# Kernel optimization log

Hardware: AMD Instinct MI355X
Metric: run time of the kernel (lower is better)

The kernel has to match this reference:

```python
import jax, jax.numpy as jnp
import numpy as np

NEG = -1e9


def setup_inputs() -> dict:
    key = jax.random.key(0)
    kq, kk, kv, ke = jax.random.split(key, 4)
    B, H, S, D = 4, 16, 2048, 64
    q = jax.random.normal(kq, (B, H, S, D), dtype=jnp.float32)
    k = jax.random.normal(kk, (B, H, S, D), dtype=jnp.float32)
    v = jax.random.normal(kv, (B, H, S, D), dtype=jnp.float32)
    event_length = jax.random.randint(ke, (B,), 0, S, dtype=jnp.int32)
    return {"q": q, "k": k, "v": v, "event_length": event_length}


def reference(q, k, v, event_length):
    B, H, S, D = q.shape
    scale = jnp.sqrt(jnp.asarray(D, dtype=jnp.float32))
    # [b,h,s,q] scores
    scores = jnp.einsum('bhsd,bhqd->bhsq', q, k) / scale
    idx = jnp.arange(S)
    el = event_length[:, None]  # [B,1]
    valid = idx[None, :] < el   # [B,S]
    # mask[b,s,q] = valid[b,s] & valid[b,q]; broadcast over heads
    mask = (valid[:, None, :, None] & valid[:, None, None, :])  # [B,1,S,S]
    scores = jnp.where(mask, scores, NEG)
    attn = jax.nn.softmax(scores, axis=-1)
    # dropout p=0.0 (eval): identity
    out = jnp.einsum('bhsq,bhqd->bhsd', attn, v)
    return out
```

## Files before the change

### kernel.cpp

```cpp
#include <hip/hip_runtime.h>
#include <hip/hip_bf16.h>


#define SQ 2048
#define DH 64
#define NBH 64
#define TK 64
#define LDE 72

typedef __attribute__((ext_vector_type(4))) float f32x4;
typedef __attribute__((ext_vector_type(8))) short bf16x8;
typedef __attribute__((ext_vector_type(4))) unsigned int u32x4;
typedef __attribute__((ext_vector_type(2))) unsigned int u32x2;

__device__ __forceinline__ unsigned int pk2(float lo, float hi) {
    __hip_bfloat162 h = __float22bfloat162_rn(float2{lo, hi});
    union { __hip_bfloat162 h; unsigned int u; } c; c.h = h;
    return c.u;
}

__global__ __launch_bounds__(256)
void meanv_k(const float* __restrict__ V, float* __restrict__ MV) {
    const int bh  = blockIdx.x >> 4;
    const int seg = blockIdx.x & 15;
    const float* vp = V + ((size_t)bh * SQ + (size_t)seg * 128) * DH;
    const int c = threadIdx.x & 15;
    const int r = threadIdx.x >> 4;
    const float* p = vp + (size_t)r * DH + c * 4;
    f32x4 s0 = *(const f32x4*)(p);
    f32x4 s1 = *(const f32x4*)(p + 16 * DH);
    f32x4 s2 = *(const f32x4*)(p + 32 * DH);
    f32x4 s3 = *(const f32x4*)(p + 48 * DH);
    s0 += *(const f32x4*)(p + 64 * DH);
    s1 += *(const f32x4*)(p + 80 * DH);
    s2 += *(const f32x4*)(p + 96 * DH);
    s3 += *(const f32x4*)(p + 112 * DH);
    f32x4 s = (s0 + s1) + (s2 + s3);
    __shared__ f32x4 red[16][16];
    red[r][c] = s;
    __syncthreads();
    if (threadIdx.x < 16) {
        f32x4 a = red[0][threadIdx.x];
        #pragma unroll
        for (int j = 1; j < 16; ++j) a += red[j][threadIdx.x];
        const float inv = 1.0f / (float)SQ;
        atomicAdd(&MV[bh * DH + threadIdx.x * 4 + 0], a[0] * inv);
        atomicAdd(&MV[bh * DH + threadIdx.x * 4 + 1], a[1] * inv);
        atomicAdd(&MV[bh * DH + threadIdx.x * 4 + 2], a[2] * inv);
        atomicAdd(&MV[bh * DH + threadIdx.x * 4 + 3], a[3] * inv);
    }
}

__global__ __launch_bounds__(256, 3)
void flash5(const float* __restrict__ Q, const float* __restrict__ K,
            const float* __restrict__ V, const int* __restrict__ EL,
            const float* __restrict__ MV, float* __restrict__ O,
            int* __restrict__ ticket) {
    const int t = threadIdx.x;

    {
        const int bh0    = blockIdx.x & (NBH - 1);
        const int qbase0 = (blockIdx.x >> 6) * 128;
        const int el0    = EL[bh0 >> 4];
        if (qbase0 >= el0) {
            float* Op = O + (size_t)bh0 * SQ * DH;
            const int c16 = t & 15, r0 = t >> 4;
            f32x4 mv = *(const f32x4*)(MV + bh0 * DH + c16 * 4);
            #pragma unroll
            for (int i = 0; i < 8; ++i)
                *(f32x4*)(Op + (size_t)(qbase0 + r0 + i * 16) * DH + c16 * 4) = mv;
        }
    }

    const int el0 = EL[0], el1 = EL[1], el2 = EL[2], el3 = EL[3];
    const int v0 = (el0 + 127) >> 7, v1 = (el1 + 127) >> 7;
    const int v2 = (el2 + 127) >> 7, v3 = (el3 + 127) >> 7;
    const int n0 = 16 * v0, n1 = n0 + 16 * v1, n2 = n1 + 16 * v2;
    const int nvalid = n2 + 16 * v3;

    __shared__ short Kb[TK][LDE];
    __shared__ short Vt[DH][LDE];
    __shared__ short Pl[4][32][LDE];
    __shared__ int item_s;

    const int wq = t >> 6, lane = t & 63, qd = lane >> 4, c = lane & 15;

    const int ksrow = t >> 2;
    const int ksdc  = t & 3;
    const int vpair = t & 31;
    const int vdg   = t >> 5;

    for (;;) {
        if (t == 0) item_s = atomicAdd(ticket, 1);
        __syncthreads();
        const int it = item_s;
        if (it >= nvalid) break;

        int b, u, vb, el;
        if      (it < n0) { b = 0; u = it;      vb = v0; el = el0; }
        else if (it < n1) { b = 1; u = it - n0; vb = v1; el = el1; }
        else if (it < n2) { b = 2; u = it - n1; vb = v2; el = el2; }
        else              { b = 3; u = it - n2; vb = v3; el = el3; }
        const int head  = u / vb;
        const int qt    = u - head * vb;
        const int bh    = b * 16 + head;
        const int qbase = qt * 128;

        const size_t base = (size_t)bh * SQ * DH;
        const float* Qp = Q + base;
        const float* Kp = K + base;
        const float* Vp = V + base;
        float* Op = O + base;

        const float sc = 0.125f * 1.44269504f;
        bf16x8 qf[2][2];
        #pragma unroll
        for (int nt = 0; nt < 2; ++nt) {
            const int row = qbase + wq * 32 + nt * 16 + c;
            #pragma unroll
            for (int kc = 0; kc < 2; ++kc) {
                const float* p = Qp + (size_t)row * DH + kc * 32 + qd * 8;
                f32x4 a  = *(const f32x4*)p;
                f32x4 bb = *(const f32x4*)(p + 4);
                u32x4 f;
                f[0] = pk2(a[0] * sc, a[1] * sc);
                f[1] = pk2(a[2] * sc, a[3] * sc);
                f[2] = pk2(bb[0] * sc, bb[1] * sc);
                f[3] = pk2(bb[2] * sc, bb[3] * sc);
                qf[nt][kc] = *(bf16x8*)&f;
            }
        }

        float l_[2] = {0.f, 0.f};
        f32x4 oacc[4][2];
        #pragma unroll
        for (int dt = 0; dt < 4; ++dt)
            #pragma unroll
            for (int nt = 0; nt < 2; ++nt)
                oacc[dt][nt] = (f32x4){0.f, 0.f, 0.f, 0.f};

        const int nkt = (el + TK - 1) / TK;

        f32x4 kg0, kg1, kg2, kg3, vg0, vg1, vg2, vg3;
        {
            const float* kp = Kp + (size_t)ksrow * DH + ksdc * 16;
            kg0 = *(const f32x4*)kp;
            kg1 = *(const f32x4*)(kp + 4);
            kg2 = *(const f32x4*)(kp + 8);
            kg3 = *(const f32x4*)(kp + 12);
            const float* vp0 = Vp + (size_t)(2 * vpair) * DH + vdg * 8;
            vg0 = *(const f32x4*)vp0;
            vg1 = *(const f32x4*)(vp0 + 4);
            vg2 = *(const f32x4*)(vp0 + DH);
            vg3 = *(const f32x4*)(vp0 + DH + 4);
        }

        for (int kt = 0; kt < nkt; ++kt) {
            const int k0 = kt * TK;

            __syncthreads();
            {
                u32x4 w0, w1;
                w0[0] = pk2(kg0[0], kg0[1]); w0[1] = pk2(kg0[2], kg0[3]);
                w0[2] = pk2(kg1[0], kg1[1]); w0[3] = pk2(kg1[2], kg1[3]);
                w1[0] = pk2(kg2[0], kg2[1]); w1[1] = pk2(kg2[2], kg2[3]);
                w1[2] = pk2(kg3[0], kg3[1]); w1[3] = pk2(kg3[2], kg3[3]);
                *(u32x4*)&Kb[ksrow][ksdc * 16]     = w0;
                *(u32x4*)&Kb[ksrow][ksdc * 16 + 8] = w1;
            }
            {
                #pragma unroll
                for (int i = 0; i < 4; ++i) {
                    *(unsigned int*)&Vt[vdg * 8 + i][2 * vpair]     = pk2(vg0[i], vg2[i]);
                    *(unsigned int*)&Vt[vdg * 8 + 4 + i][2 * vpair] = pk2(vg1[i], vg3[i]);
                }
            }
            __syncthreads();

            if (kt + 1 < nkt) {
                const int kn = k0 + TK;
                const float* kp = Kp + (size_t)(kn + ksrow) * DH + ksdc * 16;
                kg0 = *(const f32x4*)kp;
                kg1 = *(const f32x4*)(kp + 4);
                kg2 = *(const f32x4*)(kp + 8);
                kg3 = *(const f32x4*)(kp + 12);
                const float* vp0 = Vp + (size_t)(kn + 2 * vpair) * DH + vdg * 8;
                vg0 = *(const f32x4*)vp0;
                vg1 = *(const f32x4*)(vp0 + 4);
                vg2 = *(const f32x4*)(vp0 + DH);
                vg3 = *(const f32x4*)(vp0 + DH + 4);
            }

            f32x4 st[4][2];
            #pragma unroll
            for (int mt = 0; mt < 4; ++mt) {
                bf16x8 a0 = *(const bf16x8*)&Kb[mt * 16 + c][qd * 8];
                bf16x8 a1 = *(const bf16x8*)&Kb[mt * 16 + c][32 + qd * 8];
                #pragma unroll
                for (int nt = 0; nt < 2; ++nt) {
                    f32x4 acc = (f32x4){0.f, 0.f, 0.f, 0.f};
                    acc = __builtin_amdgcn_mfma_f32_16x16x32_bf16(a0, qf[nt][0], acc, 0, 0, 0);
                    acc = __builtin_amdgcn_mfma_f32_16x16x32_bf16(a1, qf[nt][1], acc, 0, 0, 0);
                    st[mt][nt] = acc;
                }
            }

            if (k0 + TK > el) {
                #pragma unroll
                for (int mt = 0; mt < 4; ++mt)
                    #pragma unroll
                    for (int r = 0; r < 4; ++r)
                        if (k0 + mt * 16 + qd * 4 + r >= el) {
                            st[mt][0][r] = -1e30f;
                            st[mt][1][r] = -1e30f;
                        }
            }

            #pragma unroll
            for (int nt = 0; nt < 2; ++nt) {
                #pragma unroll
                for (int mt = 0; mt < 4; ++mt) {
                    const float p0 = exp2f(st[mt][nt][0]);
                    const float p1 = exp2f(st[mt][nt][1]);
                    const float p2 = exp2f(st[mt][nt][2]);
                    const float p3 = exp2f(st[mt][nt][3]);
                    l_[nt] += (p0 + p1) + (p2 + p3);
                    u32x2 pw;
                    pw[0] = pk2(p0, p1);
                    pw[1] = pk2(p2, p3);
                    *(u32x2*)&Pl[wq][nt * 16 + c][mt * 16 + qd * 4] = pw;
                }
            }

            #pragma unroll
            for (int kc = 0; kc < 2; ++kc) {
                bf16x8 pb0 = *(const bf16x8*)&Pl[wq][c][kc * 32 + qd * 8];
                bf16x8 pb1 = *(const bf16x8*)&Pl[wq][16 + c][kc * 32 + qd * 8];
                #pragma unroll
                for (int dt = 0; dt < 4; ++dt) {
                    bf16x8 vf = *(const bf16x8*)&Vt[dt * 16 + c][kc * 32 + qd * 8];
                    oacc[dt][0] = __builtin_amdgcn_mfma_f32_16x16x32_bf16(vf, pb0, oacc[dt][0], 0, 0, 0);
                    oacc[dt][1] = __builtin_amdgcn_mfma_f32_16x16x32_bf16(vf, pb1, oacc[dt][1], 0, 0, 0);
                }
            }
        }

        #pragma unroll
        for (int nt = 0; nt < 2; ++nt) {
            l_[nt] += __shfl_xor(l_[nt], 16);
            l_[nt] += __shfl_xor(l_[nt], 32);
        }

        #pragma unroll
        for (int nt = 0; nt < 2; ++nt) {
            const int row = qbase + wq * 32 + nt * 16 + c;
            if (row < el) {
                const float inv = 1.0f / l_[nt];
                #pragma unroll
                for (int dt = 0; dt < 4; ++dt) {
                    f32x4 o = oacc[dt][nt];
                    o[0] *= inv; o[1] *= inv; o[2] *= inv; o[3] *= inv;
                    *(f32x4*)(Op + (size_t)row * DH + dt * 16 + qd * 4) = o;
                }
            } else {
                #pragma unroll
                for (int dt = 0; dt < 4; ++dt) {
                    f32x4 mv = *(const f32x4*)(MV + bh * DH + dt * 16 + qd * 4);
                    *(f32x4*)(Op + (size_t)row * DH + dt * 16 + qd * 4) = mv;
                }
            }
        }
    }
}

extern "C" void kernel_launch(void* const* d_in, const int* in_sizes, int n_in,
                              void* d_out, int out_size, void* d_ws, size_t ws_size,
                              hipStream_t stream) {
    const float* q  = (const float*)d_in[0];
    const float* k  = (const float*)d_in[1];
    const float* v  = (const float*)d_in[2];
    const int*   el = (const int*)d_in[3];
    float* out = (float*)d_out;
    float* mv  = (float*)d_ws;
    int*   tk  = (int*)((char*)d_ws + NBH * DH * sizeof(float));

    hipMemsetAsync(d_ws, 0, NBH * DH * sizeof(float) + 64, stream);
    meanv_k<<<dim3(NBH * 16), dim3(256), 0, stream>>>(v, mv);
    flash5<<<dim3(NBH * (SQ / 128)), dim3(256), 0, stream>>>(q, k, v, el, mv, out, tk);
}
```

Baseline: 203.3 us.

## Pre-convert K and transpose V to bf16, use single-wave blocks loading fragments directly

Adds separate pre-pass kernels that convert K to bf16 and transpose V to bf16 in a workspace, with the V mean folded into the transpose pass. The attention kernel becomes a single 64-thread wave per 32-query tile that loads MFMA fragments straight from global memory. P stays in registers instead of round-tripping through LDS, which removes all shared memory and block barriers. The cost is extra global traffic and launches for the pre-pass, loss of K/V reuse across the four waves of the old block, and a fallback path without a work ticket when the workspace is small.

```diff
diff --git a/kernel.cpp b/kernel.cpp
--- a/kernel.cpp
+++ b/kernel.cpp
@@ -6,7 +6,6 @@
 #define DH 64
 #define NBH 64
 #define TK 64
-#define LDE 72
 
 typedef __attribute__((ext_vector_type(4))) float f32x4;
 typedef __attribute__((ext_vector_type(8))) short bf16x8;
@@ -20,81 +19,95 @@
 }
 
 __global__ __launch_bounds__(256)
-void meanv_k(const float* __restrict__ V, float* __restrict__ MV) {
-    const int bh  = blockIdx.x >> 4;
-    const int seg = blockIdx.x & 15;
-    const float* vp = V + ((size_t)bh * SQ + (size_t)seg * 128) * DH;
-    const int c = threadIdx.x & 15;
-    const int r = threadIdx.x >> 4;
-    const float* p = vp + (size_t)r * DH + c * 4;
-    f32x4 s0 = *(const f32x4*)(p);
-    f32x4 s1 = *(const f32x4*)(p + 16 * DH);
-    f32x4 s2 = *(const f32x4*)(p + 32 * DH);
-    f32x4 s3 = *(const f32x4*)(p + 48 * DH);
-    s0 += *(const f32x4*)(p + 64 * DH);
-    s1 += *(const f32x4*)(p + 80 * DH);
-    s2 += *(const f32x4*)(p + 96 * DH);
-    s3 += *(const f32x4*)(p + 112 * DH);
-    f32x4 s = (s0 + s1) + (s2 + s3);
-    __shared__ f32x4 red[16][16];
-    red[r][c] = s;
-    __syncthreads();
-    if (threadIdx.x < 16) {
-        f32x4 a = red[0][threadIdx.x];
-        #pragma unroll
-        for (int j = 1; j < 16; ++j) a += red[j][threadIdx.x];
+void convert_k(const float* __restrict__ K, unsigned int* __restrict__ Kb) {
+    const size_t i = ((size_t)blockIdx.x * 256 + threadIdx.x) * 16;
+    const float* p = K + i;
+    f32x4 a = *(const f32x4*)p;
+    f32x4 b = *(const f32x4*)(p + 4);
+    f32x4 c = *(const f32x4*)(p + 8);
+    f32x4 d = *(const f32x4*)(p + 12);
+    u32x4 o0, o1;
+    o0[0] = pk2(a[0], a[1]); o0[1] = pk2(a[2], a[3]);
+    o0[2] = pk2(b[0], b[1]); o0[3] = pk2(b[2], b[3]);
+    o1[0] = pk2(c[0], c[1]); o1[1] = pk2(c[2], c[3]);
+    o1[2] = pk2(d[0], d[1]); o1[3] = pk2(d[2], d[3]);
+    *(u32x4*)(Kb + i / 2)     = o0;
+    *(u32x4*)(Kb + i / 2 + 4) = o1;
+}
+
+__global__ __launch_bounds__(256)
+void transpose_v(const float* __restrict__ V, short* __restrict__ Vt,
+                 float* __restrict__ MV) {
+    const int bh = blockIdx.x >> 5;
+    const int k0 = (blockIdx.x & 31) * 64;
+    const int t  = threadIdx.x;
+    const int kb = t & 15;
+    const int dg = t >> 4;
+    const float* vp = V + ((size_t)bh * SQ + k0 + kb * 4) * DH + dg * 4;
+    f32x4 r0 = *(const f32x4*)vp;
+    f32x4 r1 = *(const f32x4*)(vp + DH);
+    f32x4 r2 = *(const f32x4*)(vp + 2 * DH);
+    f32x4 r3 = *(const f32x4*)(vp + 3 * DH);
+    short* op = Vt + ((size_t)bh * DH + dg * 4) * SQ + k0 + kb * 4;
+    #pragma unroll
+    for (int i = 0; i < 4; ++i) {
+        u32x2 w; w[0] = pk2(r0[i], r1[i]); w[1] = pk2(r2[i], r3[i]);
+        *(u32x2*)(op + (size_t)i * SQ) = w;
+    }
+    f32x4 s = r0 + r1 + r2 + r3;
+    #pragma unroll
+    for (int d = 1; d < 16; d <<= 1) {
+        s[0] += __shfl_xor(s[0], d);
+        s[1] += __shfl_xor(s[1], d);
+        s[2] += __shfl_xor(s[2], d);
+        s[3] += __shfl_xor(s[3], d);
+    }
+    if ((t & 15) == 0) {
         const float inv = 1.0f / (float)SQ;
-        atomicAdd(&MV[bh * DH + threadIdx.x * 4 + 0], a[0] * inv);
-        atomicAdd(&MV[bh * DH + threadIdx.x * 4 + 1], a[1] * inv);
-        atomicAdd(&MV[bh * DH + threadIdx.x * 4 + 2], a[2] * inv);
-        atomicAdd(&MV[bh * DH + threadIdx.x * 4 + 3], a[3] * inv);
-    }
-}
-
-__global__ __launch_bounds__(256, 3)
-void flash5(const float* __restrict__ Q, const float* __restrict__ K,
-            const float* __restrict__ V, const int* __restrict__ EL,
+        atomicAdd(&MV[bh * DH + dg * 4 + 0], s[0] * inv);
+        atomicAdd(&MV[bh * DH + dg * 4 + 1], s[1] * inv);
+        atomicAdd(&MV[bh * DH + dg * 4 + 2], s[2] * inv);
+        atomicAdd(&MV[bh * DH + dg * 4 + 3], s[3] * inv);
+    }
+}
+
+__global__ __launch_bounds__(64, 3)
+void flash6(const float* __restrict__ Q, const short* __restrict__ Kg,
+            const short* __restrict__ Vg, const int* __restrict__ EL,
             const float* __restrict__ MV, float* __restrict__ O,
             int* __restrict__ ticket) {
-    const int t = threadIdx.x;
+    const int lane = threadIdx.x;
+    const int qd = lane >> 4, c = lane & 15;
 
     {
-        const int bh0    = blockIdx.x & (NBH - 1);
-        const int qbase0 = (blockIdx.x >> 6) * 128;
-        const int el0    = EL[bh0 >> 4];
-        if (qbase0 >= el0) {
+        const int bh0 = blockIdx.x & (NBH - 1);
+        const int qb0 = (blockIdx.x >> 6) * 32;
+        if (qb0 >= EL[bh0 >> 4]) {
             float* Op = O + (size_t)bh0 * SQ * DH;
-            const int c16 = t & 15, r0 = t >> 4;
-            f32x4 mv = *(const f32x4*)(MV + bh0 * DH + c16 * 4);
+            f32x4 mv = *(const f32x4*)(MV + bh0 * DH + c * 4);
             #pragma unroll
             for (int i = 0; i < 8; ++i)
-                *(f32x4*)(Op + (size_t)(qbase0 + r0 + i * 16) * DH + c16 * 4) = mv;
+                *(f32x4*)(Op + (size_t)(qb0 + qd + i * 4) * DH + c * 4) = mv;
         }
     }
 
     const int el0 = EL[0], el1 = EL[1], el2 = EL[2], el3 = EL[3];
-    const int v0 = (el0 + 127) >> 7, v1 = (el1 + 127) >> 7;
-    const int v2 = (el2 + 127) >> 7, v3 = (el3 + 127) >> 7;
+    const int v0 = (el0 + 31) >> 5, v1 = (el1 + 31) >> 5;
+    const int v2 = (el2 + 31) >> 5, v3 = (el3 + 31) >> 5;
     const int n0 = 16 * v0, n1 = n0 + 16 * v1, n2 = n1 + 16 * v2;
     const int nvalid = n2 + 16 * v3;
-
-    __shared__ short Kb[TK][LDE];
-    __shared__ short Vt[DH][LDE];
-    __shared__ short Pl[4][32][LDE];
-    __shared__ int item_s;
-
-    const int wq = t >> 6, lane = t & 63, qd = lane >> 4, c = lane & 15;
-
-    const int ksrow = t >> 2;
-    const int ksdc  = t & 3;
-    const int vpair = t & 31;
-    const int vdg   = t >> 5;
+    const float sc = 0.125f * 1.44269504f;
 
     for (;;) {
-        if (t == 0) item_s = atomicAdd(ticket, 1);
-        __syncthreads();
-        const int it = item_s;
-        if (it >= nvalid) break;
+        int it;
+        if (ticket) {
+            if (lane == 0) it = atomicAdd(ticket, 1);
+            it = __shfl(it, 0);
+            if (it >= nvalid) break;
+        } else {
+            it = blockIdx.x;
+            if (it >= nvalid) break;
+        }
 
         int b, u, vb, el;
         if      (it < n0) { b = 0; u = it;      vb = v0; el = el0; }
@@ -102,21 +115,19 @@
         else if (it < n2) { b = 2; u = it - n1; vb = v2; el = el2; }
         else              { b = 3; u = it - n2; vb = v3; el = el3; }
         const int head  = u / vb;
-        const int qt    = u - head * vb;
+        const int qc    = u - head * vb;
         const int bh    = b * 16 + head;
-        const int qbase = qt * 128;
-
-        const size_t base = (size_t)bh * SQ * DH;
-        const float* Qp = Q + base;
-        const float* Kp = K + base;
-        const float* Vp = V + base;
-        float* Op = O + base;
-
-        const float sc = 0.125f * 1.44269504f;
+        const int qbase = qc * 32;
+
+        const float* Qp = Q + (size_t)bh * SQ * DH;
+        const short* Kp = Kg + (size_t)bh * SQ * DH;
+        const short* Vp = Vg + (size_t)bh * DH * SQ;
+        float* Op = O + (size_t)bh * SQ * DH;
+
         bf16x8 qf[2][2];
         #pragma unroll
         for (int nt = 0; nt < 2; ++nt) {
-            const int row = qbase + wq * 32 + nt * 16 + c;
+            const int row = qbase + nt * 16 + c;
             #pragma unroll
             for (int kc = 0; kc < 2; ++kc) {
                 const float* p = Qp + (size_t)row * DH + kc * 32 + qd * 8;
@@ -140,70 +151,39 @@
                 oacc[dt][nt] = (f32x4){0.f, 0.f, 0.f, 0.f};
 
         const int nkt = (el + TK - 1) / TK;
-
-        f32x4 kg0, kg1, kg2, kg3, vg0, vg1, vg2, vg3;
-        {
-            const float* kp = Kp + (size_t)ksrow * DH + ksdc * 16;
-            kg0 = *(const f32x4*)kp;
-            kg1 = *(const f32x4*)(kp + 4);
-            kg2 = *(const f32x4*)(kp + 8);
-            kg3 = *(const f32x4*)(kp + 12);
-            const float* vp0 = Vp + (size_t)(2 * vpair) * DH + vdg * 8;
-            vg0 = *(const f32x4*)vp0;
-            vg1 = *(const f32x4*)(vp0 + 4);
-            vg2 = *(const f32x4*)(vp0 + DH);
-            vg3 = *(const f32x4*)(vp0 + DH + 4);
-        }
-
         for (int kt = 0; kt < nkt; ++kt) {
             const int k0 = kt * TK;
 
-            __syncthreads();
-            {
-                u32x4 w0, w1;
-                w0[0] = pk2(kg0[0], kg0[1]); w0[1] = pk2(kg0[2], kg0[3]);
-                w0[2] = pk2(kg1[0], kg1[1]); w0[3] = pk2(kg1[2], kg1[3]);
-                w1[0] = pk2(kg2[0], kg2[1]); w1[1] = pk2(kg2[2], kg2[3]);
-                w1[2] = pk2(kg3[0], kg3[1]); w1[3] = pk2(kg3[2], kg3[3]);
-                *(u32x4*)&Kb[ksrow][ksdc * 16]     = w0;
-                *(u32x4*)&Kb[ksrow][ksdc * 16 + 8] = w1;
-            }
-            {
-                #pragma unroll
-                for (int i = 0; i < 4; ++i) {
-                    *(unsigned int*)&Vt[vdg * 8 + i][2 * vpair]     = pk2(vg0[i], vg2[i]);
-                    *(unsigned int*)&Vt[vdg * 8 + 4 + i][2 * vpair] = pk2(vg1[i], vg3[i]);
-                }
-            }
-            __syncthreads();
-
-            if (kt + 1 < nkt) {
-                const int kn = k0 + TK;
-                const float* kp = Kp + (size_t)(kn + ksrow) * DH + ksdc * 16;
-                kg0 = *(const f32x4*)kp;
-                kg1 = *(const f32x4*)(kp + 4);
-                kg2 = *(const f32x4*)(kp + 8);
-                kg3 = *(const f32x4*)(kp + 12);
-                const float* vp0 = Vp + (size_t)(kn + 2 * vpair) * DH + vdg * 8;
-                vg0 = *(const f32x4*)vp0;
-                vg1 = *(const f32x4*)(vp0 + 4);
-                vg2 = *(const f32x4*)(vp0 + DH);
-                vg3 = *(const f32x4*)(vp0 + DH + 4);
+            bf16x8 kf[4][2];
+            #pragma unroll
+            for (int mt = 0; mt < 4; ++mt) {
+                const short* kp = Kp + (size_t)(k0 + mt * 16 + c) * DH + qd * 8;
+                kf[mt][0] = *(const bf16x8*)kp;
+                kf[mt][1] = *(const bf16x8*)(kp + 32);
+            }
+            u32x4 vf[4][2];
+            #pragma unroll
+            for (int dt = 0; dt < 4; ++dt) {
+                const short* vp = Vp + (size_t)(dt * 16 + c) * SQ + k0 + qd * 4;
+                #pragma unroll
+                for (int kc = 0; kc < 2; ++kc) {
+                    u32x2 aa = *(const u32x2*)(vp + kc * 32);
+                    u32x2 bb = *(const u32x2*)(vp + kc * 32 + 16);
+                    vf[dt][kc][0] = aa[0]; vf[dt][kc][1] = aa[1];
+                    vf[dt][kc][2] = bb[0]; vf[dt][kc][3] = bb[1];
+                }
             }
 
             f32x4 st[4][2];
             #pragma unroll
-            for (int mt = 0; mt < 4; ++mt) {
-                bf16x8 a0 = *(const bf16x8*)&Kb[mt * 16 + c][qd * 8];
-                bf16x8 a1 = *(const bf16x8*)&Kb[mt * 16 + c][32 + qd * 8];
+            for (int mt = 0; mt < 4; ++mt)
                 #pragma unroll
                 for (int nt = 0; nt < 2; ++nt) {
                     f32x4 acc = (f32x4){0.f, 0.f, 0.f, 0.f};
-                    acc = __builtin_amdgcn_mfma_f32_16x16x32_bf16(a0, qf[nt][0], acc, 0, 0, 0);
-                    acc = __builtin_amdgcn_mfma_f32_16x16x32_bf16(a1, qf[nt][1], acc, 0, 0, 0);
+                    acc = __builtin_amdgcn_mfma_f32_16x16x32_bf16(kf[mt][0], qf[nt][0], acc, 0, 0, 0);
+                    acc = __builtin_amdgcn_mfma_f32_16x16x32_bf16(kf[mt][1], qf[nt][1], acc, 0, 0, 0);
                     st[mt][nt] = acc;
                 }
-            }
 
             if (k0 + TK > el) {
                 #pragma unroll
@@ -216,6 +196,7 @@
                         }
             }
 
+            u32x2 pd[2][4];
             #pragma unroll
             for (int nt = 0; nt < 2; ++nt) {
                 #pragma unroll
@@ -225,22 +206,23 @@
                     const float p2 = exp2f(st[mt][nt][2]);
                     const float p3 = exp2f(st[mt][nt][3]);
                     l_[nt] += (p0 + p1) + (p2 + p3);
-                    u32x2 pw;
-                    pw[0] = pk2(p0, p1);
-                    pw[1] = pk2(p2, p3);
-                    *(u32x2*)&Pl[wq][nt * 16 + c][mt * 16 + qd * 4] = pw;
+                    pd[nt][mt][0] = pk2(p0, p1);
+                    pd[nt][mt][1] = pk2(p2, p3);
                 }
             }
 
             #pragma unroll
             for (int kc = 0; kc < 2; ++kc) {
-                bf16x8 pb0 = *(const bf16x8*)&Pl[wq][c][kc * 32 + qd * 8];
-                bf16x8 pb1 = *(const bf16x8*)&Pl[wq][16 + c][kc * 32 + qd * 8];
-                #pragma unroll
-                for (int dt = 0; dt < 4; ++dt) {
-                    bf16x8 vf = *(const bf16x8*)&Vt[dt * 16 + c][kc * 32 + qd * 8];
-                    oacc[dt][0] = __builtin_amdgcn_mfma_f32_16x16x32_bf16(vf, pb0, oacc[dt][0], 0, 0, 0);
-                    oacc[dt][1] = __builtin_amdgcn_mfma_f32_16x16x32_bf16(vf, pb1, oacc[dt][1], 0, 0, 0);
+                #pragma unroll
+                for (int nt = 0; nt < 2; ++nt) {
+                    u32x4 bfr;
+                    bfr[0] = pd[nt][2 * kc][0];     bfr[1] = pd[nt][2 * kc][1];
+                    bfr[2] = pd[nt][2 * kc + 1][0]; bfr[3] = pd[nt][2 * kc + 1][1];
+                    bf16x8 bb = *(bf16x8*)&bfr;
+                    #pragma unroll
+                    for (int dt = 0; dt < 4; ++dt)
+                        oacc[dt][nt] = __builtin_amdgcn_mfma_f32_16x16x32_bf16(
+                            *(bf16x8*)&vf[dt][kc], bb, oacc[dt][nt], 0, 0, 0);
                 }
             }
         }
@@ -253,7 +235,7 @@
 
         #pragma unroll
         for (int nt = 0; nt < 2; ++nt) {
-            const int row = qbase + wq * 32 + nt * 16 + c;
+            const int row = qbase + nt * 16 + c;
             if (row < el) {
                 const float inv = 1.0f / l_[nt];
                 #pragma unroll
@@ -270,6 +252,8 @@
                 }
             }
         }
+
+        if (!ticket) break;
     }
 }
 
@@ -281,10 +265,21 @@
     const float* v  = (const float*)d_in[2];
     const int*   el = (const int*)d_in[3];
     float* out = (float*)d_out;
-    float* mv  = (float*)d_ws;
-    int*   tk  = (int*)((char*)d_ws + NBH * DH * sizeof(float));
-
-    hipMemsetAsync(d_ws, 0, NBH * DH * sizeof(float) + 64, stream);
-    meanv_k<<<dim3(NBH * 16), dim3(256), 0, stream>>>(v, mv);
-    flash5<<<dim3(NBH * (SQ / 128)), dim3(256), 0, stream>>>(q, k, v, el, mv, out, tk);
-}
+
+    const size_t nelem = (size_t)NBH * SQ * DH;
+    const size_t need  = 16384 + 2 * nelem * sizeof(short);
+
+    float* mv = (float*)d_ws;
+    short* kb = (short*)((char*)d_ws + 16384);
+    short* vt = kb + nelem;
+
+    int* tk = nullptr;
+    if (ws_size >= need + 8) {
+        tk = (int*)((char*)d_ws + ((ws_size - 4) & ~(size_t)3));
+        hipMemsetAsync(tk, 0, 4, stream);
+    }
+    hipMemsetAsync(mv, 0, NBH * DH * sizeof(float), stream);
+    convert_k<<<dim3((unsigned)(nelem / (256 * 16))), dim3(256), 0, stream>>>(k, (unsigned int*)kb);
+    transpose_v<<<dim3(NBH * 32), dim3(256), 0, stream>>>(v, vt, mv);
+    flash6<<<dim3(NBH * (SQ / 32)), dim3(64), 0, stream>>>(q, kb, vt, el, mv, out, tk);
+}
```

New measurement: 356.6 us. 75.4% more time.
